# Performance work log

Hardware: AMD Instinct MI355X
Metric: run time of the kernel (lower is better)

The kernel has to match this reference:

```python
import jax, jax.numpy as jnp
import numpy as np

EPS = 1e-5


def _bn(x, g, b, axis):
    # training-mode BatchNorm1d (biased variance, eps=1e-5)
    m = x.mean(axis=axis, keepdims=True)
    v = x.var(axis=axis, keepdims=True)
    return (x - m) * jax.lax.rsqrt(v + EPS) * g + b


def _masked_softmax(s, mask):
    # softmax over each node's neighbor set; exact zeros elsewhere
    neg = jnp.finfo(s.dtype).min
    m = jnp.max(jnp.where(mask, s, neg), axis=-1, keepdims=True)
    p = jnp.where(mask, jnp.exp(s - m), 0.0)
    return p / p.sum(axis=-1, keepdims=True)


def _gcn_layer(xh, W, b, g, beta, Wa, ba, mask, apply_act):
    # xh: [H,N,Din] -> [H,N,Dout]; per-head Linear + BatchNorm over nodes
    h = jnp.einsum('hnd,hdo->hno', xh, W) + b[:, None, :]
    h = _bn(h, g[:, None, :], beta[:, None, :], axis=1)
    # dense GAT-style scores [H,N,N], LeakyReLU(0.2)
    s = jnp.einsum('hno,hom->hnm', h, Wa) + ba[:, None, :]
    s = jnp.where(s >= 0, s, 0.2 * s)
    # original detaches scores (numpy roundtrip) -> no grad through attention
    att = jax.lax.stop_gradient(_masked_softmax(s, mask))
    out = jnp.einsum('hnm,hmo->hno', att, h)
    return jax.nn.elu(out) if apply_act else out


def _forward(x, adj_mask, target_X, target,
             W0, b0, g0, beta0, Wa0, ba0,
             W1, b1, g1, beta1, Wa1, ba1,
             bng, bnb, Wp1, bp1, gp1, betap1, Wp2, bp2):
    H = W0.shape[0]
    xh = jnp.broadcast_to(x[None], (H,) + x.shape)            # replicate per head
    h = _gcn_layer(xh, W0, b0, g0, beta0, Wa0, ba0, adj_mask, True)
    h = _gcn_layer(h, W1, b1, g1, beta1, Wa1, ba1, adj_mask, False)
    out = h.sum(axis=0) / H                                    # head average [N,out]
    out = jax.nn.elu(_bn(out, bng, bnb, axis=0))
    y = jax.nn.elu(_bn(out @ Wp1 + bp1, gp1, betap1, axis=0))  # pred1
    y = y @ Wp2 + bp2                                          # pred2
    logits = y[target_X]                                       # [T,C]
    logp = jax.nn.log_softmax(logits, axis=-1)
    loss = -jnp.take_along_axis(logp, target[:, None], axis=-1).mean()
    return loss, logits


def setup_inputs() -> dict:
    key = jax.random.key(0)
    N, H, IN, H1, OUT, PRED, C, T, DEG = 4096, 4, 512, 256, 128, 64, 8, 512, 32
    ks = jax.random.split(key, 16)
    rng = np.random.default_rng(0)
    nbr = rng.integers(0, N, size=(N, DEG))
    mask = np.zeros((N, N), dtype=bool)
    mask[np.arange(N)[:, None], nbr] = True  # every row non-empty

    def lin(k, fan_in, shape):
        return jax.random.normal(k, shape, jnp.float32) / np.sqrt(fan_in)

    return {
        'x': jax.random.normal(ks[0], (N, IN), jnp.float32),
        'adj_mask': jnp.asarray(mask),
        'target_X': jax.random.randint(ks[1], (T,), 0, N),
        'target': jax.random.randint(ks[2], (T,), 0, C),
        'W0': lin(ks[3], IN, (H, IN, H1)), 'b0': jnp.zeros((H, H1)),
        'g0': jnp.ones((H, H1)), 'beta0': jnp.zeros((H, H1)),
        'Wa0': lin(ks[4], H1, (H, H1, N)), 'ba0': jnp.zeros((H, N)),
        'W1': lin(ks[5], H1, (H, H1, OUT)), 'b1': jnp.zeros((H, OUT)),
        'g1': jnp.ones((H, OUT)), 'beta1': jnp.zeros((H, OUT)),
        'Wa1': lin(ks[6], OUT, (H, OUT, N)), 'ba1': jnp.zeros((H, N)),
        'bng': jnp.ones((OUT,)), 'bnb': jnp.zeros((OUT,)),
        'Wp1': lin(ks[7], OUT, (OUT, PRED)), 'bp1': jnp.zeros((PRED,)),
        'gp1': jnp.ones((PRED,)), 'betap1': jnp.zeros((PRED,)),
        'Wp2': lin(ks[8], PRED, (PRED, C)), 'bp2': jnp.zeros((C,)),
    }


def reference(x, adj_mask, target_X, target,
              W0, b0, g0, beta0, Wa0, ba0,
              W1, b1, g1, beta1, Wa1, ba1,
              bng, bnb, Wp1, bp1, gp1, betap1, Wp2, bp2):
    return _forward(x, adj_mask, target_X, target,
                    W0, b0, g0, beta0, Wa0, ba0,
                    W1, b1, g1, beta1, Wa1, ba1,
                    bng, bnb, Wp1, bp1, gp1, betap1, Wp2, bp2)
```

## Files before the change

kernel.cpp:

```cpp
#include <hip/hip_runtime.h>
#include <hip/hip_bf16.h>
#include <math.h>

#define NN   4096
#define HH   4
#define DIN  512
#define DH1  256
#define DOUT 128
#define DPRED 64
#define NCLS 8
#define NT   512
#define NBMAX 32
#define BNCH 128

typedef __attribute__((ext_vector_type(4))) float f32x4;
typedef __attribute__((ext_vector_type(8))) short bf16x8;
typedef __attribute__((ext_vector_type(8))) unsigned short u16x8;
typedef __attribute__((ext_vector_type(4))) unsigned short u16x4;

#if defined(__has_builtin)
#if __has_builtin(__builtin_amdgcn_fdot2_f32_bf16)
#define HAVE_DOT2 1
typedef __attribute__((ext_vector_type(2))) __bf16 bf16x2_t;
#endif
#endif

#define SWZP(o) ((o) + ((o) >> 4))

__device__ __forceinline__ float b2f(unsigned short u) {
    return __uint_as_float(((unsigned)u) << 16);
}
__device__ __forceinline__ unsigned short f2b(float f) {
    __hip_bfloat16 h = __float2bfloat16(f);
    return *(unsigned short*)&h;
}

__device__ __forceinline__ float pair_dot(unsigned wpair, unsigned qpair, float acc) {
#ifdef HAVE_DOT2
    union { unsigned u; bf16x2_t v; } w, q;
    w.u = wpair; q.u = qpair;
    return __builtin_amdgcn_fdot2_f32_bf16(w.v, q.v, acc, false);
#else
    float wl = __uint_as_float(wpair << 16);
    float wh = __uint_as_float(wpair & 0xFFFF0000u);
    float ql = __uint_as_float(qpair << 16);
    float qh = __uint_as_float(qpair & 0xFFFF0000u);
    return acc + wl * ql + wh * qh;
#endif
}

__device__ __forceinline__ void gload_lds16(const __hip_bfloat16* g, __hip_bfloat16* l) {
    __builtin_amdgcn_global_load_lds(
        (__attribute__((address_space(1))) void*)(g),
        (__attribute__((address_space(3))) void*)(l), 16, 0, 0);
}

#define PREP_BLOCKS 3744
__global__ __launch_bounds__(256) void prep_k(
    const void* __restrict__ mask,
    int* __restrict__ nbr_cnt, int* __restrict__ nbr_idx,
    const float* __restrict__ x, __hip_bfloat16* __restrict__ xbf,
    const float* __restrict__ W0, __hip_bfloat16* __restrict__ W0T,
    const float* __restrict__ W1, __hip_bfloat16* __restrict__ W1T,
    const float* __restrict__ Wa0, __hip_bfloat16* __restrict__ WaT0,
    const float* __restrict__ Wa1, __hip_bfloat16* __restrict__ WaT1) {
    __shared__ float t64[64][65];
    __shared__ int md;
    int bid = blockIdx.x, tid = threadIdx.x;

    if (bid < 1024) {
        int n0 = bid * 4;
        if (tid == 0) md = 0;
        __syncthreads();
        int wave = tid >> 6, lane = tid & 63;
        int n = n0 + wave;
        const uint4* row4 = (const uint4*)((const char*)mask + (long)n * NN);
        uint4 d[4];
#pragma unroll
        for (int c = 0; c < 4; ++c) d[c] = row4[lane * 4 + c];
        unsigned accm = 0;
#pragma unroll
        for (int c = 0; c < 4; ++c) accm |= (d[c].x | d[c].y | d[c].z | d[c].w);
        if (accm & 0x0000FF00u) atomicOr(&md, 1);
        __syncthreads();
        if (md) {
            unsigned wrds[16];
#pragma unroll
            for (int c = 0; c < 4; ++c) {
                wrds[c * 4 + 0] = d[c].x; wrds[c * 4 + 1] = d[c].y;
                wrds[c * 4 + 2] = d[c].z; wrds[c * 4 + 3] = d[c].w;
            }
            int cntl = 0;
#pragma unroll
            for (int w = 0; w < 16; ++w)
#pragma unroll
                for (int j = 0; j < 4; ++j)
                    cntl += ((wrds[w] >> (8 * j)) & 0xFFu) ? 1 : 0;
            int incl = cntl;
#pragma unroll
            for (int dlt = 1; dlt < 64; dlt <<= 1) {
                int v = __shfl_up(incl, dlt);
                if (lane >= dlt) incl += v;
            }
            int pos = incl - cntl;
            int total = __shfl(incl, 63);
#pragma unroll
            for (int w = 0; w < 16; ++w)
#pragma unroll
                for (int j = 0; j < 4; ++j)
                    if ((wrds[w] >> (8 * j)) & 0xFFu) {
                        if (pos < NBMAX) nbr_idx[n * NBMAX + pos] = lane * 64 + w * 4 + j;
                        ++pos;
                    }
            if (lane == 0) nbr_cnt[n] = total > NBMAX ? NBMAX : total;
        } else {
            long base = (long)n * NN;
            const int* mw = (const int*)((const char*)mask + base * 4);
            int cnt = 0;
            unsigned long long ltmask = (1ull << lane) - 1ull;
            for (int j0 = 0; j0 < NN; j0 += 64) {
                int j = j0 + lane;
                int nz = (mw[j] != 0);
                unsigned long long bal = __ballot(nz);
                int pre = __popcll(bal & ltmask);
                if (nz) {
                    int pos = cnt + pre;
                    if (pos < NBMAX) nbr_idx[n * NBMAX + pos] = j;
                }
                cnt += __popcll(bal);
            }
            if (lane == 0) nbr_cnt[n] = cnt > NBMAX ? NBMAX : cnt;
        }
        return;
    }

    if (bid < 2048) {
        int i0 = (bid - 1024) * 512 + tid;
#pragma unroll
        for (int r = 0; r < 2; ++r) {
            int i = i0 + r * 256;
            float4 v = ((const float4*)x)[i];
            __hip_bfloat16* o = xbf + (long)i * 4;
            o[0] = __float2bfloat16(v.x); o[1] = __float2bfloat16(v.y);
            o[2] = __float2bfloat16(v.z); o[3] = __float2bfloat16(v.w);
        }
        return;
    }

    const float* in; __hip_bfloat16* outp; int R, Cc, cx, cy, b;
    if (bid < 2176) {
        int idx = bid - 2048; in = W0; outp = W0T; R = DIN; Cc = DH1;
        cx = idx & 3; cy = (idx >> 2) & 7; b = idx >> 5;
    } else if (bid < 2208) {
        int idx = bid - 2176; in = W1; outp = W1T; R = DH1; Cc = DOUT;
        cx = idx & 1; cy = (idx >> 1) & 3; b = idx >> 3;
    } else if (bid < 3232) {
        int idx = bid - 2208; in = Wa0; outp = WaT0; R = DH1; Cc = NN;
        cx = idx & 63; cy = (idx >> 6) & 3; b = idx >> 8;
    } else {
        int idx = bid - 3232; in = Wa1; outp = WaT1; R = DOUT; Cc = NN;
        cx = idx & 63; cy = (idx >> 6) & 1; b = idx >> 7;
    }
    {
        const float* ib = in + (long)b * R * Cc;
        __hip_bfloat16* ob = outp + (long)b * R * Cc;
        int c0 = cx * 64, r0 = cy * 64;
        int c4 = tid & 15, row16 = tid >> 4;
#pragma unroll
        for (int i = 0; i < 64; i += 16) {
            int r = row16 + i;
            float4 v = *(const float4*)(ib + (long)(r0 + r) * Cc + c0 + c4 * 4);
            t64[c4 * 4 + 0][r] = v.x;
            t64[c4 * 4 + 1][r] = v.y;
            t64[c4 * 4 + 2][r] = v.z;
            t64[c4 * 4 + 3][r] = v.w;
        }
        __syncthreads();
#pragma unroll
        for (int i = 0; i < 64; i += 16) {
            int c = row16 + i;
            float w0 = t64[c][c4 * 4 + 0];
            float w1 = t64[c][c4 * 4 + 1];
            float w2 = t64[c][c4 * 4 + 2];
            float w3 = t64[c][c4 * 4 + 3];
            u16x4 o4;
            o4[0] = f2b(w0); o4[1] = f2b(w1); o4[2] = f2b(w2); o4[3] = f2b(w3);
            *(u16x4*)(ob + (long)(c0 + c) * R + r0 + c4 * 4) = o4;
        }
    }
}

__global__ __launch_bounds__(256) void gemm_bf16_k(
    const __hip_bfloat16* __restrict__ A, long aBS,
    const __hip_bfloat16* __restrict__ BT, long bBS,
    __hip_bfloat16* __restrict__ C, int M, int N, int K,
    float* __restrict__ ps, float* __restrict__ ps2) {
    __shared__ __hip_bfloat16 Al[128 * 32];
    __shared__ __hip_bfloat16 Bl[128 * 32];
    __shared__ float sred[2][2][2][64];
    int b = blockIdx.z;
    const __hip_bfloat16* Ab = A + (long)b * aBS;
    const __hip_bfloat16* Bb = BT + (long)b * bBS;
    int m0 = blockIdx.x * 128, n0 = blockIdx.y * 128;
    int t = threadIdx.x;
    int lane = t & 63, wid = t >> 6;
    int wr = wid >> 1, wc = wid & 1;
    int lr = lane & 15, lg = lane >> 4;
    f32x4 acc[4][4] = {};
    for (int k0 = 0; k0 < K; k0 += 32) {
#pragma unroll
        for (int p = 0; p < 2; ++p) {
            int c = p * 256 + t;
            int row = c >> 2, cb = (c & 3) * 8;
            gload_lds16(Ab + (long)(m0 + row) * K + k0 + cb, &Al[(p * 256 + (t & 192)) * 8]);
            gload_lds16(Bb + (long)(n0 + row) * K + k0 + cb, &Bl[(p * 256 + (t & 192)) * 8]);
        }
        __syncthreads();
        bf16x8 af[4], bfr[4];
#pragma unroll
        for (int i = 0; i < 4; ++i)
            af[i] = *(const bf16x8*)&Al[(wr * 64 + i * 16 + lr) * 32 + lg * 8];
#pragma unroll
        for (int j = 0; j < 4; ++j)
            bfr[j] = *(const bf16x8*)&Bl[(wc * 64 + j * 16 + lr) * 32 + lg * 8];
#pragma unroll
        for (int i = 0; i < 4; ++i)
#pragma unroll
            for (int j = 0; j < 4; ++j)
                acc[i][j] = __builtin_amdgcn_mfma_f32_16x16x32_bf16(af[i], bfr[j], acc[i][j], 0, 0, 0);
        __syncthreads();
    }
    float s[4] = {}, s2[4] = {};
#pragma unroll
    for (int i = 0; i < 4; ++i) {
#pragma unroll
        for (int j = 0; j < 4; ++j) {
            int row = m0 + wr * 64 + i * 16 + lg * 4;
            int col = n0 + wc * 64 + j * 16 + lr;
#pragma unroll
            for (int r = 0; r < 4; ++r) {
                unsigned short rb = f2b(acc[i][j][r]);
                C[((long)b * M + row + r) * N + col] = *(__hip_bfloat16*)&rb;
                float v = b2f(rb);
                s[j] += v; s2[j] += v * v;
            }
        }
    }
#pragma unroll
    for (int j = 0; j < 4; ++j) {
#pragma unroll
        for (int d = 16; d < 64; d <<= 1) {
            s[j] += __shfl_xor(s[j], d);
            s2[j] += __shfl_xor(s2[j], d);
        }
    }
    if (lg == 0) {
#pragma unroll
        for (int j = 0; j < 4; ++j) {
            sred[0][wr][wc][j * 16 + lr] = s[j];
            sred[1][wr][wc][j * 16 + lr] = s2[j];
        }
    }
    __syncthreads();
    if (t < 128) {
        int wc2 = t >> 6, colh = t & 63;
        float ssum = sred[0][0][wc2][colh] + sred[0][1][wc2][colh];
        float s2sum = sred[1][0][wc2][colh] + sred[1][1][wc2][colh];
        long o = (long)(b * gridDim.x + blockIdx.x) * N + n0 + wc2 * 64 + colh;
        ps[o] = ssum;
        ps2[o] = s2sum;
    }
}

__global__ void gemm_aff_f32(const float* __restrict__ A, int lda,
                             const float* __restrict__ Bw, int ldb,
                             const float* __restrict__ Aaff, const float* __restrict__ Baff,
                             float* __restrict__ C, int M, int N, int K,
                             float* __restrict__ ps, float* __restrict__ ps2) {
    __shared__ float As[16][64];
    __shared__ float Bs[16][68];
    __shared__ float rs[16][64];
    __shared__ float rs2[16][64];
    int m0 = blockIdx.x * 64, n0 = blockIdx.y * 64;
    int tid = threadIdx.x;
    int tx = tid & 15, ty = tid >> 4;
    float acc[4][4] = {};
    for (int k0 = 0; k0 < K; k0 += 16) {
        {
            int r = tid >> 2, c = (tid & 3) * 4;
            float4 v = *(const float4*)(A + (long)(m0 + r) * lda + k0 + c);
            float a0 = Aaff[k0 + c + 0], b0 = Baff[k0 + c + 0];
            float a1 = Aaff[k0 + c + 1], b1 = Baff[k0 + c + 1];
            float a2 = Aaff[k0 + c + 2], b2 = Baff[k0 + c + 2];
            float a3 = Aaff[k0 + c + 3], b3 = Baff[k0 + c + 3];
            v.x = v.x * a0 + b0; v.x = v.x > 0.f ? v.x : expm1f(v.x);
            v.y = v.y * a1 + b1; v.y = v.y > 0.f ? v.y : expm1f(v.y);
            v.z = v.z * a2 + b2; v.z = v.z > 0.f ? v.z : expm1f(v.z);
            v.w = v.w * a3 + b3; v.w = v.w > 0.f ? v.w : expm1f(v.w);
            As[c + 0][r] = v.x; As[c + 1][r] = v.y; As[c + 2][r] = v.z; As[c + 3][r] = v.w;
        }
        {
            int r = tid >> 4, c = (tid & 15) * 4;
            float4 v = *(const float4*)(Bw + (long)(k0 + r) * ldb + n0 + c);
            *(float4*)&Bs[r][c] = v;
        }
        __syncthreads();
#pragma unroll
        for (int kk = 0; kk < 16; ++kk) {
            float a[4], bb[4];
#pragma unroll
            for (int i = 0; i < 4; ++i) a[i] = As[kk][ty * 4 + i];
#pragma unroll
            for (int j = 0; j < 4; ++j) bb[j] = Bs[kk][tx * 4 + j];
#pragma unroll
            for (int i = 0; i < 4; ++i)
#pragma unroll
                for (int j = 0; j < 4; ++j)
                    acc[i][j] += a[i] * bb[j];
        }
        __syncthreads();
    }
    float s[4] = {}, s2[4] = {};
#pragma unroll
    for (int i = 0; i < 4; ++i) {
        int m = m0 + ty * 4 + i;
#pragma unroll
        for (int j = 0; j < 4; ++j) {
            float v = acc[i][j];
            C[((long)m) * N + n0 + tx * 4 + j] = v;
            s[j] += v; s2[j] += v * v;
        }
    }
#pragma unroll
    for (int j = 0; j < 4; ++j) {
        rs[ty][tx * 4 + j] = s[j];
        rs2[ty][tx * 4 + j] = s2[j];
    }
    __syncthreads();
    if (tid < 64) {
        float ssum = 0.f, s2sum = 0.f;
#pragma unroll
        for (int r = 0; r < 16; ++r) { ssum += rs[r][tid]; s2sum += rs2[r][tid]; }
        long o = (long)blockIdx.x * N + n0 + tid;
        ps[o] = ssum;
        ps2[o] = s2sum;
    }
}

__global__ void avgbn_k(const float* __restrict__ l1, float* __restrict__ avg,
                        float* __restrict__ ps, float* __restrict__ ps2) {
    int c = blockIdx.x;
    int o = threadIdx.x;
    const long S = (long)NN * DOUT;
    int rows = NN / BNCH;
    float s = 0.f, s2 = 0.f;
    for (int r = 0; r < rows; ++r) {
        long i = (long)(c * rows + r) * DOUT + o;
        float v = 0.25f * (l1[i] + l1[i + S] + l1[i + 2 * S] + l1[i + 3 * S]);
        avg[i] = v;
        s += v; s2 += v * v;
    }
    ps[c * DOUT + o] = s;
    ps2[c * DOUT + o] = s2;
}

template <int D, int CH>
__global__ void bn_fin_k(const float* __restrict__ ps, const float* __restrict__ ps2,
                         int Mrows, const float* __restrict__ g, const float* __restrict__ beta,
                         float* __restrict__ Aarr, float* __restrict__ Barr) {
    int b = blockIdx.x, o = threadIdx.x;
    float s = 0.f, s2 = 0.f;
    for (int c = 0; c < CH; ++c) {
        s += ps[((b * CH) + c) * D + o];
        s2 += ps2[((b * CH) + c) * D + o];
    }
    float mean = s / Mrows;
    float var = s2 / Mrows - mean * mean;
    float inv = 1.0f / sqrtf(var + 1e-5f);
    float Ag = g[b * D + o] * inv;
    Aarr[b * D + o] = Ag;
    Barr[b * D + o] = beta[b * D + o] - mean * Ag;
}

template <int D, int OUTBF>
__global__ __launch_bounds__(256) void attn11_k(
    const __hip_bfloat16* __restrict__ h,
    const __hip_bfloat16* __restrict__ WaT,
    const float* __restrict__ ba,
    const int* __restrict__ nbr_cnt, const int* __restrict__ nbr_idx,
    const float* __restrict__ Aarr, const float* __restrict__ Barr,
    void* __restrict__ outv, int applyElu) {
    constexpr int NW = 4;
    constexpr int NG = 16;
    constexpr int EPG = D / 16;
    constexpr int PPL = EPG / 2;
    constexpr int E = D / 64;
    constexpr int KPW = NBMAX / NW;
    using u16xE = __attribute__((ext_vector_type(E))) unsigned short;

    __shared__ unsigned qp[D / 2 + D / 32 + 1];
    __shared__ float sc[NBMAX];
    __shared__ int nb[NBMAX];
    __shared__ float part[NW][D];
    __shared__ int scnt;
    int id = blockIdx.x;
    int xcd = id & 7;
    int hd = xcd >> 1;
    int n = ((id >> 3) << 1) | (xcd & 1);
    int tid = threadIdx.x;
    const unsigned short* hbu = (const unsigned short*)(h + (long)hd * NN * D);
    const unsigned short* wbu = (const unsigned short*)(WaT + (long)hd * NN * D);
    if (tid < D / 2) {
        unsigned hp = *(const unsigned*)(hbu + (long)n * D + tid * 2);
        float2 av = *(const float2*)(Aarr + hd * D + tid * 2);
        float2 bv = *(const float2*)(Barr + hd * D + tid * 2);
        float lo = b2f((unsigned short)(hp & 0xFFFFu)) * av.x + bv.x;
        float hi = b2f((unsigned short)(hp >> 16)) * av.y + bv.y;
        qp[SWZP(tid)] = (unsigned)f2b(lo) | ((unsigned)f2b(hi) << 16);
    }
    if (tid == 0) scnt = nbr_cnt[n];
    if (tid < NBMAX) nb[tid] = nbr_idx[n * NBMAX + tid];
    __syncthreads();
    int cnt = scnt;
    int wv = tid >> 6, ln = tid & 63;

    u16xE pre[KPW];
#pragma unroll
    for (int i = 0; i < KPW; ++i) {
        int kk = wv * KPW + i;
        if (kk < cnt) pre[i] = *(const u16xE*)(hbu + (long)nb[kk] * D + ln * E);
    }

    int g = tid >> 4, j = tid & 15;
#pragma unroll
    for (int k = g; k < NBMAX; k += NG) {
        if (k >= cnt) break;
        int m = nb[k];
        const unsigned* wrp = (const unsigned*)(wbu + (long)m * D) + j * PPL;
        float acc = 0.f;
#pragma unroll
        for (int c = 0; c < PPL; ++c)
            acc = pair_dot(wrp[c], qp[SWZP(j * PPL + c)], acc);
#pragma unroll
        for (int s = 8; s; s >>= 1) acc += __shfl_xor(acc, s);
        if (j == 0) {
            float sv = acc + ba[(long)hd * NN + m];
            sc[k] = sv >= 0.f ? sv : 0.2f * sv;
        }
    }
    __syncthreads();

    if (tid < 64) {
        float s = (tid < cnt) ? sc[tid] : -INFINITY;
        float mx = s;
#pragma unroll
        for (int t = 32; t; t >>= 1) mx = fmaxf(mx, __shfl_xor(mx, t));
        float p = (tid < cnt) ? expf(s - mx) : 0.f;
        float sum = p;
#pragma unroll
        for (int t = 32; t; t >>= 1) sum += __shfl_xor(sum, t);
        if (tid < cnt) sc[tid] = p / sum;
    }
    __syncthreads();

    float acc[E] = {};
#pragma unroll
    for (int i = 0; i < KPW; ++i) {
        int kk = wv * KPW + i;
        if (kk < cnt) {
            float w = sc[kk];
#pragma unroll
            for (int e = 0; e < E; ++e) acc[e] += w * b2f(pre[i][e]);
        }
    }
#pragma unroll
    for (int e = 0; e < E; ++e) part[wv][ln * E + e] = acc[e];
    __syncthreads();
    if (tid < D) {
        float v = part[0][tid] + part[1][tid] + part[2][tid] + part[3][tid];
        v = v * Aarr[hd * D + tid] + Barr[hd * D + tid];
        if (applyElu) v = v > 0.f ? v : expm1f(v);
        long oidx = ((long)hd * NN + n) * D + tid;
        if (OUTBF) ((__hip_bfloat16*)outv)[oidx] = __float2bfloat16(v);
        else ((float*)outv)[oidx] = v;
    }
}

__global__ __launch_bounds__(512) void pred2loss_k(
    const float* __restrict__ p1, const int* __restrict__ tX, const int* __restrict__ tgt,
    const float* __restrict__ Ap, const float* __restrict__ Bp,
    const float* __restrict__ Wp2, const float* __restrict__ bp2,
    float* __restrict__ out) {
    __shared__ float red[512];
    int t = threadIdx.x;
    const float* row = p1 + (long)tX[t] * DPRED;
    float v[DPRED];
#pragma unroll
    for (int j = 0; j < DPRED; ++j) {
        float u = row[j] * Ap[j] + Bp[j];
        v[j] = u > 0.f ? u : expm1f(u);
    }
    float lg[NCLS];
#pragma unroll
    for (int c = 0; c < NCLS; ++c) {
        float a = bp2[c];
        for (int j = 0; j < DPRED; ++j) a += v[j] * Wp2[j * NCLS + c];
        lg[c] = a;
        out[1 + t * NCLS + c] = a;
    }
    float mx = lg[0];
#pragma unroll
    for (int c = 1; c < NCLS; ++c) mx = fmaxf(mx, lg[c]);
    float se = 0.f;
#pragma unroll
    for (int c = 0; c < NCLS; ++c) se += expf(lg[c] - mx);
    float lse = mx + logf(se);
    int tg = tgt[t];
    float lt = lg[0];
#pragma unroll
    for (int c = 1; c < NCLS; ++c) lt = (c == tg) ? lg[c] : lt;
    red[t] = lse - lt;
    __syncthreads();
    for (int s = 256; s; s >>= 1) {
        if (t < s) red[t] += red[t + s];
        __syncthreads();
    }
    if (t == 0) out[0] = red[0] / (float)NT;
}

extern "C" void kernel_launch(void* const* d_in, const int* in_sizes, int n_in,
                              void* d_out, int out_size, void* d_ws, size_t ws_size,
                              hipStream_t stream) {
    const float* x     = (const float*)d_in[0];
    const void*  adj   = d_in[1];
    const int*   tX    = (const int*)d_in[2];
    const int*   tgt   = (const int*)d_in[3];
    const float* W0    = (const float*)d_in[4];
    const float* g0    = (const float*)d_in[6];
    const float* beta0 = (const float*)d_in[7];
    const float* Wa0   = (const float*)d_in[8];
    const float* ba0   = (const float*)d_in[9];
    const float* W1    = (const float*)d_in[10];
    const float* g1    = (const float*)d_in[12];
    const float* beta1 = (const float*)d_in[13];
    const float* Wa1   = (const float*)d_in[14];
    const float* ba1   = (const float*)d_in[15];
    const float* bng   = (const float*)d_in[16];
    const float* bnb   = (const float*)d_in[17];
    const float* Wp1   = (const float*)d_in[18];
    const float* gp1   = (const float*)d_in[20];
    const float* betap1= (const float*)d_in[21];
    const float* Wp2   = (const float*)d_in[22];
    const float* bp2   = (const float*)d_in[23];
    float* out = (float*)d_out;

    char* ws = (char*)d_ws;
    size_t off = 0;
    auto alloc = [&](size_t b) { size_t o = off; off = (off + b + 255) & ~(size_t)255; return o; };
    int*   nbr_cnt = (int*)(ws + alloc(NN * 4));
    int*   nbr_idx = (int*)(ws + alloc((size_t)NN * NBMAX * 4));
    float* ps      = (float*)(ws + alloc((size_t)HH * BNCH * DH1 * 4));
    float* ps2     = (float*)(ws + alloc((size_t)HH * BNCH * DH1 * 4));
    float* Aarr    = (float*)(ws + alloc((size_t)HH * DH1 * 4));
    float* Barr    = (float*)(ws + alloc((size_t)HH * DH1 * 4));
    __hip_bfloat16* xbf   = (__hip_bfloat16*)(ws + alloc((size_t)NN * DIN * 2));
    __hip_bfloat16* W0T   = (__hip_bfloat16*)(ws + alloc((size_t)HH * DH1 * DIN * 2));
    __hip_bfloat16* W1T   = (__hip_bfloat16*)(ws + alloc((size_t)HH * DOUT * DH1 * 2));
    __hip_bfloat16* WaT0b = (__hip_bfloat16*)(ws + alloc((size_t)HH * NN * DH1 * 2));
    __hip_bfloat16* WaT1b = (__hip_bfloat16*)(ws + alloc((size_t)HH * NN * DOUT * 2));
    __hip_bfloat16* h0bf  = (__hip_bfloat16*)(ws + alloc((size_t)HH * NN * DH1 * 2));
    __hip_bfloat16* g1bf  = (__hip_bfloat16*)(ws + alloc((size_t)HH * NN * DH1 * 2));
    __hip_bfloat16* h1bf  = (__hip_bfloat16*)(ws + alloc((size_t)HH * NN * DOUT * 2));
    float* l1out = (float*)(ws + alloc((size_t)HH * NN * DOUT * 4));
    float* avg   = (float*)(ws + alloc((size_t)NN * DOUT * 4));
    float* p1    = (float*)(ws + alloc((size_t)NN * DPRED * 4));

    prep_k<<<PREP_BLOCKS, 256, 0, stream>>>(adj, nbr_cnt, nbr_idx, x, xbf,
                                            W0, W0T, W1, W1T, Wa0, WaT0b, Wa1, WaT1b);

    gemm_bf16_k<<<dim3(NN / 128, DH1 / 128, HH), 256, 0, stream>>>(
        xbf, 0L, W0T, (long)DH1 * DIN, h0bf, NN, DH1, DIN, ps, ps2);
    bn_fin_k<DH1, 32><<<HH, DH1, 0, stream>>>(ps, ps2, NN, g0, beta0, Aarr, Barr);
    attn11_k<DH1, 1><<<NN * HH, 256, 0, stream>>>(
        h0bf, WaT0b, ba0, nbr_cnt, nbr_idx, Aarr, Barr, g1bf, 1);

    gemm_bf16_k<<<dim3(NN / 128, 1, HH), 256, 0, stream>>>(
        g1bf, (long)NN * DH1, W1T, (long)DOUT * DH1, h1bf, NN, DOUT, DH1, ps, ps2);
    bn_fin_k<DOUT, 32><<<HH, DOUT, 0, stream>>>(ps, ps2, NN, g1, beta1, Aarr, Barr);
    attn11_k<DOUT, 0><<<NN * HH, 256, 0, stream>>>(
        h1bf, WaT1b, ba1, nbr_cnt, nbr_idx, Aarr, Barr, l1out, 0);

    avgbn_k<<<BNCH, DOUT, 0, stream>>>(l1out, avg, ps, ps2);
    bn_fin_k<DOUT, BNCH><<<1, DOUT, 0, stream>>>(ps, ps2, NN, bng, bnb, Aarr, Barr);

    gemm_aff_f32<<<dim3(NN / 64, 1, 1), 256, 0, stream>>>(
        avg, DOUT, Wp1, DPRED, Aarr, Barr, p1, NN, DPRED, DOUT, ps, ps2);
    bn_fin_k<DPRED, 64><<<1, DPRED, 0, stream>>>(ps, ps2, NN, gp1, betap1, Aarr, Barr);

    pred2loss_k<<<1, 512, 0, stream>>>(p1, tX, tgt, Aarr, Barr, Wp2, bp2, out);
}
```

Before: 194.9 us.

## Fuse BatchNorm finalize into producer kernels via last-block atomic counter

Removes the four separate bn_fin_k launches by having the last-finishing block of each GEMM/reduction kernel (detected with a threadfence plus atomic counter) compute the BN scale/shift arrays. A separate Ap2/Bp2 buffer is added because gemm_aff_f32 reads Aarr/Barr while producing the next stats. This saves kernel launch overhead and inter-kernel gaps. In exchange it adds a memset, one serialized tail block per kernel, and fence/atomic costs.

Result: slower. 272.8 us (+39.9%).

```diff
diff --git a/kernel.cpp b/kernel.cpp
--- a/kernel.cpp
+++ b/kernel.cpp
@@ -53,6 +53,22 @@
     __builtin_amdgcn_global_load_lds(
         (__attribute__((address_space(1))) void*)(g),
         (__attribute__((address_space(3))) void*)(l), 16, 0, 0);
+}
+
+__device__ __forceinline__ void bn_finalize_col(
+    const float* ps, const float* ps2, int CH, int N, int b, int o, int Mrows,
+    const float* g, const float* beta, float* Aarr, float* Barr) {
+    float s = 0.f, s2 = 0.f;
+    for (int c = 0; c < CH; ++c) {
+        s += ps[(long)(b * CH + c) * N + o];
+        s2 += ps2[(long)(b * CH + c) * N + o];
+    }
+    float mean = s / Mrows;
+    float var = s2 / Mrows - mean * mean;
+    float inv = 1.0f / sqrtf(var + 1e-5f);
+    float Ag = g[b * N + o] * inv;
+    Aarr[b * N + o] = Ag;
+    Barr[b * N + o] = beta[b * N + o] - mean * Ag;
 }
 
 #define PREP_BLOCKS 3744
@@ -179,12 +195,11 @@
 #pragma unroll
         for (int i = 0; i < 64; i += 16) {
             int c = row16 + i;
-            float w0 = t64[c][c4 * 4 + 0];
-            float w1 = t64[c][c4 * 4 + 1];
-            float w2 = t64[c][c4 * 4 + 2];
-            float w3 = t64[c][c4 * 4 + 3];
             u16x4 o4;
-            o4[0] = f2b(w0); o4[1] = f2b(w1); o4[2] = f2b(w2); o4[3] = f2b(w3);
+            o4[0] = f2b(t64[c][c4 * 4 + 0]);
+            o4[1] = f2b(t64[c][c4 * 4 + 1]);
+            o4[2] = f2b(t64[c][c4 * 4 + 2]);
+            o4[3] = f2b(t64[c][c4 * 4 + 3]);
             *(u16x4*)(ob + (long)(c0 + c) * R + r0 + c4 * 4) = o4;
         }
     }
@@ -194,10 +209,14 @@
     const __hip_bfloat16* __restrict__ A, long aBS,
     const __hip_bfloat16* __restrict__ BT, long bBS,
     __hip_bfloat16* __restrict__ C, int M, int N, int K,
-    float* __restrict__ ps, float* __restrict__ ps2) {
+    float* __restrict__ ps, float* __restrict__ ps2,
+    const float* __restrict__ g, const float* __restrict__ beta,
+    float* __restrict__ Aarr, float* __restrict__ Barr,
+    int* __restrict__ ctr) {
     __shared__ __hip_bfloat16 Al[128 * 32];
     __shared__ __hip_bfloat16 Bl[128 * 32];
     __shared__ float sred[2][2][2][64];
+    __shared__ int isLast;
     int b = blockIdx.z;
     const __hip_bfloat16* Ab = A + (long)b * aBS;
     const __hip_bfloat16* Bb = BT + (long)b * bBS;
@@ -270,17 +289,31 @@
         ps[o] = ssum;
         ps2[o] = s2sum;
     }
+    __threadfence();
+    __syncthreads();
+    if (t == 0)
+        isLast = (atomicAdd(&ctr[b], 1) == (int)(gridDim.x * gridDim.y) - 1);
+    __syncthreads();
+    if (!isLast) return;
+    __threadfence();
+    int CH = gridDim.x;
+    for (int o = t; o < N; o += 256)
+        bn_finalize_col(ps, ps2, CH, N, b, o, M, g, beta, Aarr, Barr);
 }
 
 __global__ void gemm_aff_f32(const float* __restrict__ A, int lda,
                              const float* __restrict__ Bw, int ldb,
                              const float* __restrict__ Aaff, const float* __restrict__ Baff,
                              float* __restrict__ C, int M, int N, int K,
-                             float* __restrict__ ps, float* __restrict__ ps2) {
+                             float* __restrict__ ps, float* __restrict__ ps2,
+                             const float* __restrict__ g, const float* __restrict__ beta,
+                             float* __restrict__ Aout, float* __restrict__ Bout,
+                             int* __restrict__ ctr) {
     __shared__ float As[16][64];
     __shared__ float Bs[16][68];
     __shared__ float rs[16][64];
     __shared__ float rs2[16][64];
+    __shared__ int isLast;
     int m0 = blockIdx.x * 64, n0 = blockIdx.y * 64;
     int tid = threadIdx.x;
     int tx = tid & 15, ty = tid >> 4;
@@ -345,10 +378,24 @@
         ps[o] = ssum;
         ps2[o] = s2sum;
     }
+    __threadfence();
+    __syncthreads();
+    if (tid == 0)
+        isLast = (atomicAdd(ctr, 1) == (int)(gridDim.x * gridDim.y) - 1);
+    __syncthreads();
+    if (!isLast) return;
+    __threadfence();
+    int CH = gridDim.x;
+    for (int o = tid; o < N; o += 256)
+        bn_finalize_col(ps, ps2, CH, N, 0, o, M, g, beta, Aout, Bout);
 }
 
 __global__ void avgbn_k(const float* __restrict__ l1, float* __restrict__ avg,
-                        float* __restrict__ ps, float* __restrict__ ps2) {
+                        float* __restrict__ ps, float* __restrict__ ps2,
+                        const float* __restrict__ g, const float* __restrict__ beta,
+                        float* __restrict__ Aarr, float* __restrict__ Barr,
+                        int* __restrict__ ctr) {
+    __shared__ int isLast;
     int c = blockIdx.x;
     int o = threadIdx.x;
     const long S = (long)NN * DOUT;
@@ -362,24 +409,13 @@
     }
     ps[c * DOUT + o] = s;
     ps2[c * DOUT + o] = s2;
-}
-
-template <int D, int CH>
-__global__ void bn_fin_k(const float* __restrict__ ps, const float* __restrict__ ps2,
-                         int Mrows, const float* __restrict__ g, const float* __restrict__ beta,
-                         float* __restrict__ Aarr, float* __restrict__ Barr) {
-    int b = blockIdx.x, o = threadIdx.x;
-    float s = 0.f, s2 = 0.f;
-    for (int c = 0; c < CH; ++c) {
-        s += ps[((b * CH) + c) * D + o];
-        s2 += ps2[((b * CH) + c) * D + o];
-    }
-    float mean = s / Mrows;
-    float var = s2 / Mrows - mean * mean;
-    float inv = 1.0f / sqrtf(var + 1e-5f);
-    float Ag = g[b * D + o] * inv;
-    Aarr[b * D + o] = Ag;
-    Barr[b * D + o] = beta[b * D + o] - mean * Ag;
+    __threadfence();
+    __syncthreads();
+    if (o == 0) isLast = (atomicAdd(ctr, 1) == BNCH - 1);
+    __syncthreads();
+    if (!isLast) return;
+    __threadfence();
+    bn_finalize_col(ps, ps2, BNCH, DOUT, 0, o, NN, g, beta, Aarr, Barr);
 }
 
 template <int D, int OUTBF>
@@ -557,12 +593,15 @@
     char* ws = (char*)d_ws;
     size_t off = 0;
     auto alloc = [&](size_t b) { size_t o = off; off = (off + b + 255) & ~(size_t)255; return o; };
+    int*   ctr     = (int*)(ws + alloc(128));
     int*   nbr_cnt = (int*)(ws + alloc(NN * 4));
     int*   nbr_idx = (int*)(ws + alloc((size_t)NN * NBMAX * 4));
     float* ps      = (float*)(ws + alloc((size_t)HH * BNCH * DH1 * 4));
     float* ps2     = (float*)(ws + alloc((size_t)HH * BNCH * DH1 * 4));
     float* Aarr    = (float*)(ws + alloc((size_t)HH * DH1 * 4));
     float* Barr    = (float*)(ws + alloc((size_t)HH * DH1 * 4));
+    float* Ap2     = (float*)(ws + alloc((size_t)DPRED * 4));
+    float* Bp2     = (float*)(ws + alloc((size_t)DPRED * 4));
     __hip_bfloat16* xbf   = (__hip_bfloat16*)(ws + alloc((size_t)NN * DIN * 2));
     __hip_bfloat16* W0T   = (__hip_bfloat16*)(ws + alloc((size_t)HH * DH1 * DIN * 2));
     __hip_bfloat16* W1T   = (__hip_bfloat16*)(ws + alloc((size_t)HH * DOUT * DH1 * 2));
@@ -575,27 +614,28 @@
     float* avg   = (float*)(ws + alloc((size_t)NN * DOUT * 4));
     float* p1    = (float*)(ws + alloc((size_t)NN * DPRED * 4));
 
+    hipMemsetAsync(ctr, 0, 128, stream);
+
     prep_k<<<PREP_BLOCKS, 256, 0, stream>>>(adj, nbr_cnt, nbr_idx, x, xbf,
                                             W0, W0T, W1, W1T, Wa0, WaT0b, Wa1, WaT1b);
 
-    gemm_bf16_k<<<dim3(NN / 128, DH1 / 128, HH), 256, 0, stream>>>(
-        xbf, 0L, W0T, (long)DH1 * DIN, h0bf, NN, DH1, DIN, ps, ps2);
-    bn_fin_k<DH1, 32><<<HH, DH1, 0, stream>>>(ps, ps2, NN, g0, beta0, Aarr, Barr);
+    gemm_bf16_k<<<dim3(32, DH1 / 128, HH), 256, 0, stream>>>(
+        xbf, 0L, W0T, (long)DH1 * DIN, h0bf, NN, DH1, DIN, ps, ps2,
+        g0, beta0, Aarr, Barr, ctr + 0);
     attn11_k<DH1, 1><<<NN * HH, 256, 0, stream>>>(
         h0bf, WaT0b, ba0, nbr_cnt, nbr_idx, Aarr, Barr, g1bf, 1);
 
-    gemm_bf16_k<<<dim3(NN / 128, 1, HH), 256, 0, stream>>>(
-        g1bf, (long)NN * DH1, W1T, (long)DOUT * DH1, h1bf, NN, DOUT, DH1, ps, ps2);
-    bn_fin_k<DOUT, 32><<<HH, DOUT, 0, stream>>>(ps, ps2, NN, g1, beta1, Aarr, Barr);
+    gemm_bf16_k<<<dim3(32, 1, HH), 256, 0, stream>>>(
+        g1bf, (long)NN * DH1, W1T, (long)DOUT * DH1, h1bf, NN, DOUT, DH1, ps, ps2,
+        g1, beta1, Aarr, Barr, ctr + 8);
     attn11_k<DOUT, 0><<<NN * HH, 256, 0, stream>>>(
         h1bf, WaT1b, ba1, nbr_cnt, nbr_idx, Aarr, Barr, l1out, 0);
 
-    avgbn_k<<<BNCH, DOUT, 0, stream>>>(l1out, avg, ps, ps2);
-    bn_fin_k<DOUT, BNCH><<<1, DOUT, 0, stream>>>(ps, ps2, NN, bng, bnb, Aarr, Barr);
+    avgbn_k<<<BNCH, DOUT, 0, stream>>>(l1out, avg, ps, ps2, bng, bnb, Aarr, Barr, ctr + 16);
 
     gemm_aff_f32<<<dim3(NN / 64, 1, 1), 256, 0, stream>>>(
-        avg, DOUT, Wp1, DPRED, Aarr, Barr, p1, NN, DPRED, DOUT, ps, ps2);
-    bn_fin_k<DPRED, 64><<<1, DPRED, 0, stream>>>(ps, ps2, NN, gp1, betap1, Aarr, Barr);
-
-    pred2loss_k<<<1, 512, 0, stream>>>(p1, tX, tgt, Aarr, Barr, Wp2, bp2, out);
-}
+        avg, DOUT, Wp1, DPRED, Aarr, Barr, p1, NN, DPRED, DOUT, ps, ps2,
+        gp1, betap1, Ap2, Bp2, ctr + 17);
+
+    pred2loss_k<<<1, 512, 0, stream>>>(p1, tX, tgt, Ap2, Bp2, Wp2, bp2, out);
+}
```
